# Kernel optimization log

Measured on AMD Instinct MI355X. Metric: run time of the kernel, lower is better.

The kernel has to match this reference:

```python
import jax, jax.numpy as jnp
import numpy as np

B, C, H, W = 4, 512, 64, 64
CQ = C // 8  # 64 channels for each of query/key projections


def conv1x1(t, w, b):
    # t: [B, Cin, H, W], w: [Cout, Cin], b: [Cout]
    return jnp.einsum('bchw,oc->bohw', t, w) + b[None, :, None, None]


def setup_inputs() -> dict:
    key = jax.random.key(0)
    ks = jax.random.split(key, 12)
    s = 0.05
    return {
        'x':   jax.random.normal(ks[0], (B, C, H, W), jnp.float32),
        'dep': jax.random.normal(ks[1], (B, C, H, W), jnp.float32),
        'wq':  jax.random.normal(ks[2], (CQ, C), jnp.float32) * s,
        'bq':  jnp.zeros((CQ,), jnp.float32),
        'wqd': jax.random.normal(ks[3], (CQ, C), jnp.float32) * s,
        'bqd': jnp.zeros((CQ,), jnp.float32),
        'wk':  jax.random.normal(ks[4], (CQ, C), jnp.float32) * s,
        'bk':  jnp.zeros((CQ,), jnp.float32),
        'wkd': jax.random.normal(ks[5], (CQ, C), jnp.float32) * s,
        'bkd': jnp.zeros((CQ,), jnp.float32),
        'wv':  jax.random.normal(ks[6], (C, C), jnp.float32) * s,
        'bv':  jnp.zeros((C,), jnp.float32),
        'gamma': jnp.full((1,), 0.5, jnp.float32),
    }


def reference(x, dep, wq, bq, wqd, bqd, wk, bk, wkd, bkd, wv, bv, gamma):
    b, c, h, w = x.shape
    n = h * w
    # concatenated RGB+depth query/key projections: [B, 2*CQ, N]
    q = jnp.concatenate([conv1x1(x, wq, bq), conv1x1(dep, wqd, bqd)], axis=1).reshape(b, -1, n)
    k = jnp.concatenate([conv1x1(x, wk, bk), conv1x1(dep, wkd, bkd)], axis=1).reshape(b, -1, n)
    # energy[b, i, j] = sum_d q[b, d, i] * k[b, d, j]  -> [B, N, N]
    energy = jnp.einsum('bdi,bdj->bij', q, k)
    attn = jax.nn.softmax(energy, axis=-1)
    v = conv1x1(x, wv, bv).reshape(b, c, n)  # [B, C, N]
    # out[b, c, i] = sum_j v[b, c, j] * attn[b, i, j]
    out = jnp.einsum('bcj,bij->bci', v, attn).reshape(b, c, h, w)
    return gamma.reshape(()) * out + x
```

## Files before the change

kernel.cpp:

```cpp
#include <hip/hip_runtime.h>


typedef __attribute__((ext_vector_type(8))) short bf16x8;
typedef __attribute__((ext_vector_type(4))) float f32x4;

__device__ __forceinline__ float bf2f(unsigned short u) {
  return __builtin_bit_cast(float, (unsigned int)u << 16);
}
__device__ __forceinline__ unsigned short f2bf(float f) {
  unsigned int u = __builtin_bit_cast(unsigned int, f);
  u = u + 0x7fffu + ((u >> 16) & 1u);
  return (unsigned short)(u >> 16);
}
__device__ __forceinline__ float bflo(unsigned int u) {
  return __builtin_bit_cast(float, u << 16);
}

__device__ __forceinline__ void gld16(const char* g, char* l) {
  __builtin_amdgcn_global_load_lds(
      (const __attribute__((address_space(1))) unsigned int*)g,
      (__attribute__((address_space(3))) unsigned int*)l, 16, 0, 0);
}

__device__ __forceinline__ int detect_fp32_mode(const void* xv) {
  const unsigned int* p = (const unsigned int*)xv;
  const int lane = threadIdx.x & 63;
  const unsigned int w0 = p[lane];
  const unsigned int w1 = p[64 + lane];
  int cnt = 0;
  const unsigned short us[4] = {
      (unsigned short)(w0 & 0xffffu), (unsigned short)(w0 >> 16),
      (unsigned short)(w1 & 0xffffu), (unsigned short)(w1 >> 16)};
#pragma unroll
  for (int h = 0; h < 4; ++h) {
    const float a = fabsf(bf2f(us[h]));
    cnt += (a > 9.0e-13f && a < 32.0f) ? 1 : 0;
  }
#pragma unroll
  for (int mm = 32; mm >= 1; mm >>= 1) cnt += __shfl_xor(cnt, mm, 64);
  return cnt < 220;
}

__global__ __launch_bounds__(256) void prep_kernel(
    const void* wq, const void* bq, const void* wqd, const void* bqd,
    const void* wk, const void* bk, const void* wkd, const void* bkd,
    const void* wv, const void* bv, const void* gam, const void* x,
    unsigned short* __restrict__ Whi, unsigned short* __restrict__ Wlo,
    float* __restrict__ Bcat, float* __restrict__ gamF)
{
  const int fp32mode = detect_fp32_mode(x);
  const int row = blockIdx.x;
  const void* src; const void* bsrc; int srow;
  if (row < 64)       { src = wq;  bsrc = bq;  srow = row; }
  else if (row < 128) { src = wqd; bsrc = bqd; srow = row - 64; }
  else if (row < 192) { src = wk;  bsrc = bk;  srow = row - 128; }
  else if (row < 256) { src = wkd; bsrc = bkd; srow = row - 192; }
  else                { src = wv;  bsrc = bv;  srow = row - 256; }
  for (int c = threadIdx.x; c < 512; c += 256) {
    const float v = fp32mode ? ((const float*)src)[(size_t)srow * 512 + c]
                             : bf2f(((const unsigned short*)src)[(size_t)srow * 512 + c]);
    const unsigned short h = f2bf(v);
    Whi[(size_t)row * 512 + c] = h;
    Wlo[(size_t)row * 512 + c] = f2bf(v - bf2f(h));
  }
  if (threadIdx.x == 0) {
    Bcat[row] = fp32mode ? ((const float*)bsrc)[srow]
                         : bf2f(((const unsigned short*)bsrc)[srow]);
    if (row == 0)
      gamF[0] = fp32mode ? ((const float*)gam)[0]
                         : bf2f(((const unsigned short*)gam)[0]);
  }
}

__global__ __launch_bounds__(256) void convert_kernel(
    const void* __restrict__ x, const void* __restrict__ dep,
    unsigned short* __restrict__ Xst)
{
  __shared__ float XT[512][36];
  const int fp32mode = detect_fp32_mode(x);
  const int tid = threadIdx.x;
  const int bid = blockIdx.x;
  const int src = bid & 1, t = (bid >> 1) & 127, b = bid >> 8;
  const int n0 = t * 32;
  const void* s = src ? dep : x;
  const int crow = tid >> 3;
  const int nf   = (tid & 7) * 4;

  float v[16][4];
  if (fp32mode) {
    const float* sp = (const float*)s;
#pragma unroll
    for (int r = 0; r < 16; ++r) {
      const int c = crow + r * 32;
      const float4 f4 = *(const float4*)(sp + (((size_t)b * 512 + c) << 12) + n0 + nf);
      v[r][0] = f4.x; v[r][1] = f4.y; v[r][2] = f4.z; v[r][3] = f4.w;
    }
  } else {
    const unsigned short* sp = (const unsigned short*)s;
#pragma unroll
    for (int r = 0; r < 16; ++r) {
      const int c = crow + r * 32;
      const uint2 u2 = *(const uint2*)(sp + (((size_t)b * 512 + c) << 12) + n0 + nf);
      v[r][0] = bflo(u2.x & 0xffffu); v[r][1] = bflo(u2.x >> 16);
      v[r][2] = bflo(u2.y & 0xffffu); v[r][3] = bflo(u2.y >> 16);
    }
  }
  __builtin_amdgcn_sched_barrier(0);
#pragma unroll
  for (int r = 0; r < 16; ++r) {
    const int c = crow + r * 32;
#pragma unroll
    for (int k = 0; k < 4; ++k) XT[c][nf + k] = v[r][k];
  }
  __syncthreads();

  const int n  = tid & 31;
  const int cg = tid >> 5;
  char* pb = (char*)Xst + ((((size_t)b * 128 + t) * 2 + src) << 16);
  const unsigned swz = (unsigned)(n & 7) << 4;
#pragma unroll
  for (int g = 0; g < 8; ++g) {
    unsigned short hi8[8], lo8[8];
#pragma unroll
    for (int i = 0; i < 8; ++i) {
      const float vv = XT[cg * 64 + g * 8 + i][n];
      const unsigned short h = f2bf(vv);
      hi8[i] = h;
      lo8[i] = f2bf(vv - bf2f(h));
    }
    const unsigned off = ((unsigned)(n * 1024 + 2 * (cg * 64 + g * 8))) ^ swz;
    *(uint4*)(pb + off)         = *(const uint4*)hi8;
    *(uint4*)(pb + 32768 + off) = *(const uint4*)lo8;
  }
}

__device__ __forceinline__ void gtile(
    const unsigned short* __restrict__ Whi, const unsigned short* __restrict__ Wlo,
    const float* bsh, const char* __restrict__ XL, int fp32mode,
    int wrow0, int kind, int d0, int b, int t, int n0, int l15, int quad,
    unsigned short* __restrict__ Qhi, unsigned short* __restrict__ Qlo,
    unsigned short* __restrict__ Kst, unsigned short* __restrict__ Vst)
{
  f32x4 A0, A1, B0, B1, C0, C1;
#pragma unroll
  for (int r = 0; r < 4; ++r) {
    A0[r] = A1[r] = bsh[wrow0 + quad * 4 + r];
    B0[r] = B1[r] = C0[r] = C1[r] = 0.f;
  }
  const unsigned short* wh_p = Whi + (size_t)(wrow0 + l15) * 512 + quad * 8;
  const unsigned short* wl_p = Wlo + (size_t)(wrow0 + l15) * 512 + quad * 8;
  const unsigned base0 = (unsigned)(l15 * 1024 + quad * 16);
  const unsigned swz   = (unsigned)(l15 & 7) << 4;

  bf16x8 hc = *(const bf16x8*)(wh_p);
  bf16x8 lc;
  if (fp32mode) lc = *(const bf16x8*)(wl_p);

#pragma unroll 2
  for (int ks = 0; ks < 16; ++ks) {
    bf16x8 hn, ln;
    if (ks < 15) {
      hn = *(const bf16x8*)(wh_p + (ks + 1) * 32);
      if (fp32mode) ln = *(const bf16x8*)(wl_p + (ks + 1) * 32);
    }
    const unsigned o0 = (base0 + ks * 64) ^ swz;
    const unsigned o1 = o0 + 16384;
    const bf16x8 b0 = *(const bf16x8*)(XL + o0);
    const bf16x8 b1 = *(const bf16x8*)(XL + o1);
    A0 = __builtin_amdgcn_mfma_f32_16x16x32_bf16(hc, b0, A0, 0, 0, 0);
    A1 = __builtin_amdgcn_mfma_f32_16x16x32_bf16(hc, b1, A1, 0, 0, 0);
    if (fp32mode) {
      const bf16x8 c0 = *(const bf16x8*)(XL + 32768 + o0);
      const bf16x8 c1 = *(const bf16x8*)(XL + 32768 + o1);
      B0 = __builtin_amdgcn_mfma_f32_16x16x32_bf16(hc, c0, B0, 0, 0, 0);
      C0 = __builtin_amdgcn_mfma_f32_16x16x32_bf16(lc, b0, C0, 0, 0, 0);
      B1 = __builtin_amdgcn_mfma_f32_16x16x32_bf16(hc, c1, B1, 0, 0, 0);
      C1 = __builtin_amdgcn_mfma_f32_16x16x32_bf16(lc, b1, C1, 0, 0, 0);
    }
    if (ks < 15) { hc = hn; if (fp32mode) lc = ln; }
  }

  const f32x4 a0 = fp32mode ? (A0 + B0) + C0 : A0;
  const f32x4 a1 = fp32mode ? (A1 + B1) + C1 : A1;
#pragma unroll
  for (int ns = 0; ns < 2; ++ns) {
    const f32x4 acc = ns ? a1 : a0;
    const int j = ns * 16 + l15;
    if (kind <= 1) {
      ushort4 h, l;
#pragma unroll
      for (int r = 0; r < 4; ++r) {
        const float f = acc[r];
        const unsigned short hh = f2bf(f);
        ((unsigned short*)&h)[r] = hh;
        ((unsigned short*)&l)[r] = f2bf(f - bf2f(hh));
      }
      if (kind == 0) {
        const size_t base = (((size_t)b << 12) + n0 + j) * 128 + d0 + quad * 4;
        *(ushort4*)(Qhi + base) = h;
        *(ushort4*)(Qlo + base) = l;
      } else {
        char* tb = (char*)Kst + (((size_t)b * 128 + t) << 14);
        const unsigned off =
            ((unsigned)(j * 256 + (d0 + quad * 4) * 2)) ^ ((unsigned)(j & 7) << 4);
        *(ushort4*)(tb + off) = h;
        *(ushort4*)(tb + 8192 + off) = l;
      }
    } else {
      char* tb = (char*)Vst + (((size_t)b * 128 + t) << 15);
#pragma unroll
      for (int r = 0; r < 4; ++r) {
        const int c = d0 + quad * 4 + r;
        const unsigned off =
            ((unsigned)(c * 64 + j * 2)) ^ ((unsigned)(c & 7) << 4);
        *(unsigned short*)(tb + off) = f2bf(acc[r]);
      }
    }
  }
}

__global__ __launch_bounds__(512, 4) void gemm_kernel(
    const void* __restrict__ x,
    const unsigned short* __restrict__ Whi, const unsigned short* __restrict__ Wlo,
    const float* __restrict__ Bcat, const unsigned short* __restrict__ Xst,
    unsigned short* __restrict__ Qhi, unsigned short* __restrict__ Qlo,
    unsigned short* __restrict__ Kst, unsigned short* __restrict__ Vst)
{
  __shared__ char XL[65536];
  __shared__ float bsh[768];
  const int fp32mode = detect_fp32_mode(x);
  const int tid  = threadIdx.x;
  const int lane = tid & 63;
  const int w    = tid >> 6;
  const int l15  = lane & 15;
  const int quad = lane >> 4;
  const int t  = blockIdx.x;
  const int b  = blockIdx.y;
  const int n0 = t * 32;

  for (int i = tid; i < 768; i += 512) bsh[i] = Bcat[i];

  const char* xsrc = (const char*)Xst + ((((size_t)b * 128 + t) * 2 + 0) << 16);
  const char* dsrc = xsrc + 65536;

#pragma unroll
  for (int i = 0; i < 8; ++i) {
    const int c8 = w + i * 8;
    gld16(xsrc + c8 * 1024 + lane * 16, XL + c8 * 1024);
  }
  __syncthreads();

  for (int i = 0; i < 5; ++i) {
    const int rt = w + i * 8;
    int wrow0, kind, d0;
    if (rt < 4)      { wrow0 = rt * 16;             kind = 0; d0 = rt * 16; }
    else if (rt < 8) { wrow0 = 128 + (rt - 4) * 16; kind = 1; d0 = (rt - 4) * 16; }
    else             { wrow0 = 256 + (rt - 8) * 16; kind = 2; d0 = (rt - 8) * 16; }
    gtile(Whi, Wlo, bsh, XL, fp32mode, wrow0, kind, d0, b, t, n0, l15, quad,
          Qhi, Qlo, Kst, Vst);
  }
  __syncthreads();

#pragma unroll
  for (int i = 0; i < 8; ++i) {
    const int c8 = w + i * 8;
    gld16(dsrc + c8 * 1024 + lane * 16, XL + c8 * 1024);
  }
  __syncthreads();

  {
    const int kind  = (w < 4) ? 0 : 1;
    const int wrow0 = (w < 4) ? 64 + w * 16 : 192 + (w - 4) * 16;
    const int d0    = 64 + (w & 3) * 16;
    gtile(Whi, Wlo, bsh, XL, fp32mode, wrow0, kind, d0, b, t, n0, l15, quad,
          Qhi, Qlo, Kst, Vst);
  }
}

__device__ __forceinline__ void stage_X(
    const void* __restrict__ src, int fp32mode, int b, int n0,
    int cbase, int nn,
    unsigned short* __restrict__ Xhi, unsigned short* __restrict__ Xlo)
{
  float v[8][4];
  if (fp32mode) {
    const float* s = (const float*)src;
#pragma unroll
    for (int r = 0; r < 8; ++r) {
      const int c = cbase + r * 64;
      const float4 f4 = *(const float4*)(s + (((size_t)b * 512 + c) << 12) + n0 + nn);
      v[r][0] = f4.x; v[r][1] = f4.y; v[r][2] = f4.z; v[r][3] = f4.w;
    }
  } else {
    const unsigned short* s = (const unsigned short*)src;
#pragma unroll
    for (int r = 0; r < 8; ++r) {
      const int c = cbase + r * 64;
      const uint2 u2 = *(const uint2*)(s + (((size_t)b * 512 + c) << 12) + n0 + nn);
      v[r][0] = bflo(u2.x & 0xffffu); v[r][1] = bflo(u2.x >> 16);
      v[r][2] = bflo(u2.y & 0xffffu); v[r][3] = bflo(u2.y >> 16);
    }
  }
  __builtin_amdgcn_sched_barrier(0);
#pragma unroll
  for (int r = 0; r < 8; ++r) {
    const int c = cbase + r * 64;
#pragma unroll
    for (int k = 0; k < 4; ++k) {
      const unsigned short h = f2bf(v[r][k]);
      Xhi[(nn + k) * 522 + c] = h;
      Xlo[(nn + k) * 522 + c] = f2bf(v[r][k] - bf2f(h));
    }
  }
}

__device__ __forceinline__ void do_tile_c(
    const unsigned short* __restrict__ Whi, const unsigned short* __restrict__ Wlo,
    const float* bsh,
    const unsigned short* Xhi, const unsigned short* Xlo, int fp32mode,
    int wrow0, int kind, int d0,
    int l15, int quad,
    char* __restrict__ QT, char* __restrict__ KT, char* __restrict__ VT)
{
  f32x4 A0, A1, B0, B1, C0, C1;
#pragma unroll
  for (int r = 0; r < 4; ++r) {
    A0[r] = A1[r] = bsh[wrow0 + quad * 4 + r];
    B0[r] = B1[r] = C0[r] = C1[r] = 0.f;
  }
  const unsigned short* wh_p = Whi + (size_t)(wrow0 + l15) * 512 + quad * 8;
  const unsigned short* wl_p = Wlo + (size_t)(wrow0 + l15) * 512 + quad * 8;
  const unsigned short* x0h = Xhi + l15 * 522 + quad * 8;
  const unsigned short* x1h = Xhi + (16 + l15) * 522 + quad * 8;
  const unsigned short* x0l = Xlo + l15 * 522 + quad * 8;
  const unsigned short* x1l = Xlo + (16 + l15) * 522 + quad * 8;

  bf16x8 hc = *(const bf16x8*)(wh_p);
  bf16x8 lc;
  if (fp32mode) lc = *(const bf16x8*)(wl_p);

#pragma unroll 2
  for (int ks = 0; ks < 16; ++ks) {
    bf16x8 hn, ln;
    if (ks < 15) {
      hn = *(const bf16x8*)(wh_p + (ks + 1) * 32);
      if (fp32mode) ln = *(const bf16x8*)(wl_p + (ks + 1) * 32);
    }
    const int o = ks * 32;
    const bf16x8 b0 = *(const bf16x8*)(x0h + o);
    const bf16x8 b1 = *(const bf16x8*)(x1h + o);
    A0 = __builtin_amdgcn_mfma_f32_16x16x32_bf16(hc, b0, A0, 0, 0, 0);
    A1 = __builtin_amdgcn_mfma_f32_16x16x32_bf16(hc, b1, A1, 0, 0, 0);
    if (fp32mode) {
      const bf16x8 c0 = *(const bf16x8*)(x0l + o);
      const bf16x8 c1 = *(const bf16x8*)(x1l + o);
      B0 = __builtin_amdgcn_mfma_f32_16x16x32_bf16(hc, c0, B0, 0, 0, 0);
      C0 = __builtin_amdgcn_mfma_f32_16x16x32_bf16(lc, b0, C0, 0, 0, 0);
      B1 = __builtin_amdgcn_mfma_f32_16x16x32_bf16(hc, c1, B1, 0, 0, 0);
      C1 = __builtin_amdgcn_mfma_f32_16x16x32_bf16(lc, b1, C1, 0, 0, 0);
    }
    if (ks < 15) { hc = hn; if (fp32mode) lc = ln; }
  }

  const f32x4 a0 = fp32mode ? (A0 + B0) + C0 : A0;
  const f32x4 a1 = fp32mode ? (A1 + B1) + C1 : A1;
#pragma unroll
  for (int ns = 0; ns < 2; ++ns) {
    const f32x4 acc = ns ? a1 : a0;
    const int n = ns * 16 + l15;
    if (kind <= 1) {
      ushort4 h, l;
#pragma unroll
      for (int r = 0; r < 4; ++r) {
        const float f = acc[r];
        const unsigned short hh = f2bf(f);
        ((unsigned short*)&h)[r] = hh;
        ((unsigned short*)&l)[r] = f2bf(f - bf2f(hh));
      }
      const unsigned lin = (unsigned)(n * 256 + (d0 + quad * 4) * 2);
      if (kind == 0) {
        *(ushort4*)(QT + lin) = h;
        *(ushort4*)(QT + 8192 + lin) = l;
      } else {
        const unsigned off = lin ^ ((unsigned)(n & 7) << 4);
        *(ushort4*)(KT + off) = h;
        *(ushort4*)(KT + 8192 + off) = l;
      }
    } else {
#pragma unroll
      for (int r = 0; r < 4; ++r) {
        const int c = d0 + quad * 4 + r;
        const unsigned off =
            ((unsigned)(c * 64 + n * 2)) ^ ((unsigned)(c & 7) << 4);
        *(unsigned short*)(VT + off) = f2bf(acc[r]);
      }
    }
  }
}

__global__ __launch_bounds__(512, 2) void proj_kernel(
    const void* __restrict__ x, const void* __restrict__ dep,
    const unsigned short* __restrict__ Whi, const unsigned short* __restrict__ Wlo,
    const float* __restrict__ Bcat,
    unsigned short* __restrict__ Qhi, unsigned short* __restrict__ Qlo,
    unsigned short* __restrict__ Kst, unsigned short* __restrict__ Vst)
{
  __shared__ unsigned short Xhi[32 * 522];
  __shared__ unsigned short Xlo[32 * 522];
  __shared__ char QT[16384];
  __shared__ char KT[16384];
  __shared__ char VT[32768];
  __shared__ float bsh[768];
  const int fp32mode = detect_fp32_mode(x);
  const int tid  = threadIdx.x;
  const int lane = tid & 63;
  const int w    = tid >> 6;
  const int l15  = lane & 15;
  const int quad = lane >> 4;
  const int b  = blockIdx.y;
  const int cbase = tid >> 3;
  const int nn    = (tid & 7) * 4;

  for (int i = tid; i < 768; i += 512) bsh[i] = Bcat[i];

  for (int rep = 0; rep < 2; ++rep) {
    const int t  = blockIdx.x + rep * 64;
    const int n0 = t * 32;
    stage_X(x, fp32mode, b, n0, cbase, nn, Xhi, Xlo);
    __syncthreads();
    for (int rt = w; rt < 40; rt += 8) {
      int wrow0, kind, d0;
      if (rt < 4)      { wrow0 = rt * 16;             kind = 0; d0 = rt * 16; }
      else if (rt < 8) { wrow0 = 128 + (rt - 4) * 16; kind = 1; d0 = (rt - 4) * 16; }
      else             { wrow0 = 256 + (rt - 8) * 16; kind = 2; d0 = (rt - 8) * 16; }
      do_tile_c(Whi, Wlo, bsh, Xhi, Xlo, fp32mode, wrow0, kind, d0,
                l15, quad, QT, KT, VT);
    }
    __syncthreads();
    {
      char* vdst = (char*)Vst + (((size_t)b * 128 + t) << 15);
#pragma unroll
      for (int i = 0; i < 4; ++i) {
        const int off = i * 8192 + tid * 16;
        *(uint4*)(vdst + off) = *(const uint4*)(VT + off);
      }
    }
    stage_X(dep, fp32mode, b, n0, cbase, nn, Xhi, Xlo);
    __syncthreads();
    {
      const int rt = w;
      const int kind  = (rt < 4) ? 0 : 1;
      const int wrow0 = (rt < 4) ? 64 + rt * 16 : 192 + (rt - 4) * 16;
      const int d0    = 64 + (rt & 3) * 16;
      do_tile_c(Whi, Wlo, bsh, Xhi, Xlo, fp32mode, wrow0, kind, d0,
                l15, quad, QT, KT, VT);
    }
    __syncthreads();
    {
      char* kdst = (char*)Kst + (((size_t)b * 128 + t) << 14);
#pragma unroll
      for (int i = 0; i < 2; ++i) {
        const int off = i * 8192 + tid * 16;
        *(uint4*)(kdst + off) = *(const uint4*)(KT + off);
      }
      const size_t qoff = ((((size_t)b << 12) + (size_t)t * 32) * 128) * 2;
      *(uint4*)((char*)Qhi + qoff + tid * 16) = *(const uint4*)(QT + tid * 16);
      *(uint4*)((char*)Qlo + qoff + tid * 16) = *(const uint4*)(QT + 8192 + tid * 16);
    }
    __syncthreads();
  }
}

__global__ __launch_bounds__(768, 3) void attn_kernel(
    const unsigned short* __restrict__ Qhi, const unsigned short* __restrict__ Qlo,
    const unsigned short* __restrict__ Kst, const unsigned short* __restrict__ Vst,
    const void* __restrict__ x, const float* __restrict__ gamF,
    void* __restrict__ outp)
{
  __shared__ char KL[2][16384];
  __shared__ char VL[2][32768];
  __shared__ unsigned short P[2][64][40];
  __shared__ float lstat[2][4][16];

  const int fp32mode = detect_fp32_mode(x);
  const int tid  = threadIdx.x;
  const int lane = tid & 63;
  const int w    = tid >> 6;
  const int l15  = lane & 15;
  const int quad = lane >> 4;
  const int id   = blockIdx.x;
  const int b    = (id >> 1) & 3;
  const int n0   = (((id >> 3) << 1) | (id & 1)) * 64;

  asm volatile("" :: "v"(fp32mode) : "memory");

  const char* Kb = (const char*)Kst + (((size_t)b * 128) << 14);
  const char* Vb = (const char*)Vst + (((size_t)b * 128) << 15);

  if (w < 4) {
    const int ihE = w >> 1;
    const int jt  = w & 1;
    bf16x8 qh[2][4], ql[2][4];
#pragma unroll
    for (int itq = 0; itq < 2; ++itq) {
      const size_t qb =
          (((size_t)b << 12) + n0 + ihE * 32 + itq * 16 + l15) * 128 + quad * 8;
#pragma unroll
      for (int ds = 0; ds < 4; ++ds) {
        qh[itq][ds] = *(const bf16x8*)(Qhi + qb + ds * 32);
        ql[itq][ds] = *(const bf16x8*)(Qlo + qb + ds * 32);
      }
    }
#pragma unroll
    for (int ch = 0; ch < 4; ++ch) {
      const int c = w + ch * 4;
      gld16(Kb + c * 1024 + lane * 16, &KL[0][c * 1024]);
    }
    float lpart[2] = {0.f, 0.f};

    for (int t = 0; t <= 128; ++t) {
      asm volatile("s_waitcnt vmcnt(0) lgkmcnt(0)" ::: "memory");
      __builtin_amdgcn_sched_barrier(0);
      __builtin_amdgcn_s_barrier();
      __builtin_amdgcn_sched_barrier(0);
      if (t < 128) {
        const int cur = t & 1;
        if (t < 127) {
          const char* src = Kb + ((size_t)(t + 1) << 14);
#pragma unroll
          for (int ch = 0; ch < 4; ++ch) {
            const int c = w + ch * 4;
            gld16(src + c * 1024 + lane * 16, &KL[cur ^ 1][c * 1024]);
          }
        }
        __builtin_amdgcn_sched_barrier(0);
        const int row = jt * 16 + l15;
        const unsigned rsw = (unsigned)(row & 7) << 4;
        const char* kb = &KL[cur][0];
        bf16x8 kh[4], kl[4];
#pragma unroll
        for (int ds = 0; ds < 4; ++ds) {
          const unsigned off = ((unsigned)(row * 256 + quad * 16 + ds * 64)) ^ rsw;
          kh[ds] = *(const bf16x8*)(kb + off);
          kl[ds] = *(const bf16x8*)(kb + 8192 + off);
        }
        f32x4 ea[2], eb[2], ec[2];
#pragma unroll
        for (int itq = 0; itq < 2; ++itq) {
          ea[itq] = (f32x4){0.f, 0.f, 0.f, 0.f};
          eb[itq] = (f32x4){0.f, 0.f, 0.f, 0.f};
          ec[itq] = (f32x4){0.f, 0.f, 0.f, 0.f};
        }
        __builtin_amdgcn_s_setprio(1);
#pragma unroll
        for (int ds = 0; ds < 4; ++ds)
#pragma unroll
          for (int itq = 0; itq < 2; ++itq) {
            ea[itq] = __builtin_amdgcn_mfma_f32_16x16x32_bf16(kh[ds], qh[itq][ds], ea[itq], 0, 0, 0);
            eb[itq] = __builtin_amdgcn_mfma_f32_16x16x32_bf16(kh[ds], ql[itq][ds], eb[itq], 0, 0, 0);
            ec[itq] = __builtin_amdgcn_mfma_f32_16x16x32_bf16(kl[ds], qh[itq][ds], ec[itq], 0, 0, 0);
          }
        __builtin_amdgcn_s_setprio(0);
#pragma unroll
        for (int itq = 0; itq < 2; ++itq) {
          const f32x4 e = (ea[itq] + eb[itq]) + ec[itq];
          const float p0 = __expf(e[0] - 32.0f);
          const float p1 = __expf(e[1] - 32.0f);
          const float p2 = __expf(e[2] - 32.0f);
          const float p3 = __expf(e[3] - 32.0f);
          const unsigned short u0 = f2bf(p0), u1 = f2bf(p1);
          const unsigned short u2 = f2bf(p2), u3 = f2bf(p3);
          lpart[itq] += (bf2f(u0) + bf2f(u1)) + (bf2f(u2) + bf2f(u3));
          unsigned int* dst = (unsigned int*)
              (&P[cur][ihE * 32 + itq * 16 + l15][jt * 16 + quad * 4]);
          dst[0] = (unsigned int)u0 | ((unsigned int)u1 << 16);
          dst[1] = (unsigned int)u2 | ((unsigned int)u3 << 16);
        }
      }
    }
#pragma unroll
    for (int itq = 0; itq < 2; ++itq) {
      float lp = lpart[itq];
      lp += __shfl_xor(lp, 16, 64);
      lp += __shfl_xor(lp, 32, 64);
      if (quad == 0) lstat[jt][ihE * 2 + itq][l15] = lp;
    }
    __syncthreads();
    return;
  }

  const int wv = w - 4;
#pragma unroll
  for (int k = 0; k < 4; ++k) {
    const int c = wv * 4 + k;
    gld16(Vb + c * 1024 + lane * 16, &VL[0][c * 1024]);
  }
  f32x4 acc[4][4];
#pragma unroll
  for (int ct = 0; ct < 4; ++ct)
#pragma unroll
    for (int itv = 0; itv < 4; ++itv) acc[ct][itv] = (f32x4){0.f, 0.f, 0.f, 0.f};

  for (int t = 0; t <= 128; ++t) {
    if (t <= 127)
      asm volatile("s_waitcnt vmcnt(4)" ::: "memory");
    else
      asm volatile("s_waitcnt vmcnt(0)" ::: "memory");
    __builtin_amdgcn_sched_barrier(0);
    __builtin_amdgcn_s_barrier();
    __builtin_amdgcn_sched_barrier(0);
    if (t >= 1) {
      const int pb = (t - 1) & 1;
      bf16x8 pf[4];
#pragma unroll
      for (int itv = 0; itv < 4; ++itv)
        pf[itv] = *(const bf16x8*)(&P[pb][itv * 16 + l15][quad * 8]);
      const char* vb = &VL[pb][0];
      __builtin_amdgcn_s_setprio(1);
#pragma unroll
      for (int ct = 0; ct < 4; ++ct) {
        const int c = wv * 64 + ct * 16 + l15;
        const unsigned off =
            ((unsigned)(c * 64 + quad * 16)) ^ ((unsigned)(c & 7) << 4);
        const bf16x8 va = *(const bf16x8*)(vb + off);
#pragma unroll
        for (int itv = 0; itv < 4; ++itv)
          acc[ct][itv] = __builtin_amdgcn_mfma_f32_16x16x32_bf16(va, pf[itv], acc[ct][itv], 0, 0, 0);
      }
      __builtin_amdgcn_s_setprio(0);
      __builtin_amdgcn_sched_barrier(0);
    }
    if (t < 127) {
      const char* src = Vb + ((size_t)(t + 1) << 15);
#pragma unroll
      for (int k = 0; k < 4; ++k) {
        const int c = wv * 4 + k;
        gld16(src + c * 1024 + lane * 16, &VL[(t + 1) & 1][c * 1024]);
      }
    }
  }
  __syncthreads();

  const float gv = gamF[0];
  float sc[4];
#pragma unroll
  for (int itv = 0; itv < 4; ++itv) {
    const float l = lstat[0][itv][l15] + lstat[1][itv][l15];
    sc[itv] = gv / l;
  }
#pragma unroll
  for (int ct = 0; ct < 4; ++ct)
#pragma unroll
    for (int r = 0; r < 4; ++r) {
      const int c_g = wv * 64 + ct * 16 + quad * 4 + r;
      const size_t brow = ((size_t)b * 512 + c_g) << 12;
#pragma unroll
      for (int itv = 0; itv < 4; ++itv) {
        const size_t addr = brow + n0 + itv * 16 + l15;
        const float o = sc[itv] * acc[ct][itv][r];
        if (fp32mode) {
          ((float*)outp)[addr] = o + ((const float*)x)[addr];
        } else {
          ((unsigned short*)outp)[addr] =
              f2bf(o + bf2f(((const unsigned short*)x)[addr]));
        }
      }
    }
}

extern "C" void kernel_launch(void* const* d_in, const int* in_sizes, int n_in,
                              void* d_out, int out_size, void* d_ws, size_t ws_size,
                              hipStream_t stream) {
  const void* x    = d_in[0];
  const void* dep  = d_in[1];
  const void* wq   = d_in[2];
  const void* bq   = d_in[3];
  const void* wqd  = d_in[4];
  const void* bqd  = d_in[5];
  const void* wk   = d_in[6];
  const void* bk   = d_in[7];
  const void* wkd  = d_in[8];
  const void* bkd  = d_in[9];
  const void* wv   = d_in[10];
  const void* bv   = d_in[11];
  const void* gam  = d_in[12];

  unsigned short* Whi = (unsigned short*)d_ws;
  unsigned short* Wlo = Whi + (size_t)768 * 512;
  float* Bcat = (float*)(Wlo + (size_t)768 * 512);
  float* gamF = Bcat + 768;
  unsigned short* Qhi = (unsigned short*)((char*)d_ws + ((size_t)2 << 20));
  unsigned short* Qlo = (unsigned short*)((char*)d_ws + ((size_t)6 << 20));
  unsigned short* Kst = (unsigned short*)((char*)d_ws + ((size_t)10 << 20));
  unsigned short* Vst = (unsigned short*)((char*)d_ws + ((size_t)18 << 20));
  unsigned short* Xst = (unsigned short*)((char*)d_ws + ((size_t)36 << 20));

  prep_kernel<<<768, 256, 0, stream>>>(wq, bq, wqd, bqd, wk, bk, wkd, bkd,
                                       wv, bv, gam, x, Whi, Wlo, Bcat, gamF);
  if (ws_size >= ((size_t)100 << 20)) {
    convert_kernel<<<1024, 256, 0, stream>>>(x, dep, Xst);
    gemm_kernel<<<dim3(128, 4), 512, 0, stream>>>(x, Whi, Wlo, Bcat, Xst,
                                                  Qhi, Qlo, Kst, Vst);
  } else {
    proj_kernel<<<dim3(64, 4), 512, 0, stream>>>(x, dep, Whi, Wlo, Bcat,
                                                 Qhi, Qlo, Kst, Vst);
  }
  attn_kernel<<<256, 768, 0, stream>>>(Qhi, Qlo, Kst, Vst, x, gamF, d_out);
}
```

Before: 396.3 us.

## Read K/V tiles directly from global memory and split energy work across eight waves

Drops the LDS double-buffered K and V staging (global_load_lds) and has each wave load its K and V fragments straight from global memory, depending on the cache. The energy stage now runs on eight producer waves, each handling 16 query rows instead of 32, and the block grows to 1024 threads. The aim is to free LDS, lower per-wave register pressure and give more parallelism to the softmax/energy producer. The cost is redundant global/L2 traffic, since every wave re-reads K and V, and load latency that is no longer hidden by prefetch. Launch bounds of (1024,4) may also force register spills.

```diff
diff --git a/kernel.cpp b/kernel.cpp
--- a/kernel.cpp
+++ b/kernel.cpp
@@ -471,14 +471,12 @@
   }
 }
 
-__global__ __launch_bounds__(768, 3) void attn_kernel(
+__global__ __launch_bounds__(1024, 4) void attn_kernel(
     const unsigned short* __restrict__ Qhi, const unsigned short* __restrict__ Qlo,
     const unsigned short* __restrict__ Kst, const unsigned short* __restrict__ Vst,
     const void* __restrict__ x, const float* __restrict__ gamF,
     void* __restrict__ outp)
 {
-  __shared__ char KL[2][16384];
-  __shared__ char VL[2][32768];
   __shared__ unsigned short P[2][64][40];
   __shared__ float lstat[2][4][16];
 
@@ -492,51 +490,33 @@
   const int b    = (id >> 1) & 3;
   const int n0   = (((id >> 3) << 1) | (id & 1)) * 64;
 
-  asm volatile("" :: "v"(fp32mode) : "memory");
-
   const char* Kb = (const char*)Kst + (((size_t)b * 128) << 14);
   const char* Vb = (const char*)Vst + (((size_t)b * 128) << 15);
 
-  if (w < 4) {
-    const int ihE = w >> 1;
-    const int jt  = w & 1;
-    bf16x8 qh[2][4], ql[2][4];
-#pragma unroll
-    for (int itq = 0; itq < 2; ++itq) {
+  if (w < 8) {
+    const int rg = w >> 1;
+    const int jt = w & 1;
+    bf16x8 qh[4], ql[4];
+    {
       const size_t qb =
-          (((size_t)b << 12) + n0 + ihE * 32 + itq * 16 + l15) * 128 + quad * 8;
+          (((size_t)b << 12) + n0 + rg * 16 + l15) * 128 + quad * 8;
 #pragma unroll
       for (int ds = 0; ds < 4; ++ds) {
-        qh[itq][ds] = *(const bf16x8*)(Qhi + qb + ds * 32);
-        ql[itq][ds] = *(const bf16x8*)(Qlo + qb + ds * 32);
-      }
-    }
-#pragma unroll
-    for (int ch = 0; ch < 4; ++ch) {
-      const int c = w + ch * 4;
-      gld16(Kb + c * 1024 + lane * 16, &KL[0][c * 1024]);
-    }
-    float lpart[2] = {0.f, 0.f};
+        qh[ds] = *(const bf16x8*)(Qhi + qb + ds * 32);
+        ql[ds] = *(const bf16x8*)(Qlo + qb + ds * 32);
+      }
+    }
+    const int row = jt * 16 + l15;
+    const unsigned rsw = (unsigned)(row & 7) << 4;
+    float lpart = 0.f;
 
     for (int t = 0; t <= 128; ++t) {
-      asm volatile("s_waitcnt vmcnt(0) lgkmcnt(0)" ::: "memory");
+      asm volatile("s_waitcnt lgkmcnt(0)" ::: "memory");
       __builtin_amdgcn_sched_barrier(0);
       __builtin_amdgcn_s_barrier();
       __builtin_amdgcn_sched_barrier(0);
       if (t < 128) {
-        const int cur = t & 1;
-        if (t < 127) {
-          const char* src = Kb + ((size_t)(t + 1) << 14);
-#pragma unroll
-          for (int ch = 0; ch < 4; ++ch) {
-            const int c = w + ch * 4;
-            gld16(src + c * 1024 + lane * 16, &KL[cur ^ 1][c * 1024]);
-          }
-        }
-        __builtin_amdgcn_sched_barrier(0);
-        const int row = jt * 16 + l15;
-        const unsigned rsw = (unsigned)(row & 7) << 4;
-        const char* kb = &KL[cur][0];
+        const char* kb = Kb + ((size_t)t << 14);
         bf16x8 kh[4], kl[4];
 #pragma unroll
         for (int ds = 0; ds < 4; ++ds) {
@@ -544,99 +524,77 @@
           kh[ds] = *(const bf16x8*)(kb + off);
           kl[ds] = *(const bf16x8*)(kb + 8192 + off);
         }
-        f32x4 ea[2], eb[2], ec[2];
-#pragma unroll
-        for (int itq = 0; itq < 2; ++itq) {
-          ea[itq] = (f32x4){0.f, 0.f, 0.f, 0.f};
-          eb[itq] = (f32x4){0.f, 0.f, 0.f, 0.f};
-          ec[itq] = (f32x4){0.f, 0.f, 0.f, 0.f};
+        __builtin_amdgcn_sched_barrier(0);
+        f32x4 ea = (f32x4){0.f, 0.f, 0.f, 0.f};
+        f32x4 eb = (f32x4){0.f, 0.f, 0.f, 0.f};
+        f32x4 ec = (f32x4){0.f, 0.f, 0.f, 0.f};
+        __builtin_amdgcn_s_setprio(1);
+#pragma unroll
+        for (int ds = 0; ds < 4; ++ds) {
+          ea = __builtin_amdgcn_mfma_f32_16x16x32_bf16(kh[ds], qh[ds], ea, 0, 0, 0);
+          eb = __builtin_amdgcn_mfma_f32_16x16x32_bf16(kh[ds], ql[ds], eb, 0, 0, 0);
+          ec = __builtin_amdgcn_mfma_f32_16x16x32_bf16(kl[ds], qh[ds], ec, 0, 0, 0);
         }
-        __builtin_amdgcn_s_setprio(1);
-#pragma unroll
-        for (int ds = 0; ds < 4; ++ds)
-#pragma unroll
-          for (int itq = 0; itq < 2; ++itq) {
-            ea[itq] = __builtin_amdgcn_mfma_f32_16x16x32_bf16(kh[ds], qh[itq][ds], ea[itq], 0, 0, 0);
-            eb[itq] = __builtin_amdgcn_mfma_f32_16x16x32_bf16(kh[ds], ql[itq][ds], eb[itq], 0, 0, 0);
-            ec[itq] = __builtin_amdgcn_mfma_f32_16x16x32_bf16(kl[ds], qh[itq][ds], ec[itq], 0, 0, 0);
-          }
         __builtin_amdgcn_s_setprio(0);
-#pragma unroll
-        for (int itq = 0; itq < 2; ++itq) {
-          const f32x4 e = (ea[itq] + eb[itq]) + ec[itq];
-          const float p0 = __expf(e[0] - 32.0f);
-          const float p1 = __expf(e[1] - 32.0f);
-          const float p2 = __expf(e[2] - 32.0f);
-          const float p3 = __expf(e[3] - 32.0f);
-          const unsigned short u0 = f2bf(p0), u1 = f2bf(p1);
-          const unsigned short u2 = f2bf(p2), u3 = f2bf(p3);
-          lpart[itq] += (bf2f(u0) + bf2f(u1)) + (bf2f(u2) + bf2f(u3));
-          unsigned int* dst = (unsigned int*)
-              (&P[cur][ihE * 32 + itq * 16 + l15][jt * 16 + quad * 4]);
-          dst[0] = (unsigned int)u0 | ((unsigned int)u1 << 16);
-          dst[1] = (unsigned int)u2 | ((unsigned int)u3 << 16);
-        }
-      }
-    }
-#pragma unroll
-    for (int itq = 0; itq < 2; ++itq) {
-      float lp = lpart[itq];
+        const f32x4 e = (ea + eb) + ec;
+        const float p0 = __expf(e[0] - 32.0f);
+        const float p1 = __expf(e[1] - 32.0f);
+        const float p2 = __expf(e[2] - 32.0f);
+        const float p3 = __expf(e[3] - 32.0f);
+        const unsigned short u0 = f2bf(p0), u1 = f2bf(p1);
+        const unsigned short u2 = f2bf(p2), u3 = f2bf(p3);
+        lpart += (bf2f(u0) + bf2f(u1)) + (bf2f(u2) + bf2f(u3));
+        unsigned int* dst = (unsigned int*)
+            (&P[t & 1][rg * 16 + l15][jt * 16 + quad * 4]);
+        dst[0] = (unsigned int)u0 | ((unsigned int)u1 << 16);
+        dst[1] = (unsigned int)u2 | ((unsigned int)u3 << 16);
+      }
+    }
+    {
+      float lp = lpart;
       lp += __shfl_xor(lp, 16, 64);
       lp += __shfl_xor(lp, 32, 64);
-      if (quad == 0) lstat[jt][ihE * 2 + itq][l15] = lp;
+      if (quad == 0) lstat[jt][rg][l15] = lp;
     }
     __syncthreads();
     return;
   }
 
-  const int wv = w - 4;
-#pragma unroll
-  for (int k = 0; k < 4; ++k) {
-    const int c = wv * 4 + k;
-    gld16(Vb + c * 1024 + lane * 16, &VL[0][c * 1024]);
-  }
+  const int wv = w - 8;
   f32x4 acc[4][4];
 #pragma unroll
   for (int ct = 0; ct < 4; ++ct)
 #pragma unroll
     for (int itv = 0; itv < 4; ++itv) acc[ct][itv] = (f32x4){0.f, 0.f, 0.f, 0.f};
 
+  const unsigned vswz = (unsigned)(l15 & 7) << 4;
   for (int t = 0; t <= 128; ++t) {
-    if (t <= 127)
-      asm volatile("s_waitcnt vmcnt(4)" ::: "memory");
-    else
-      asm volatile("s_waitcnt vmcnt(0)" ::: "memory");
+    asm volatile("s_waitcnt lgkmcnt(0)" ::: "memory");
     __builtin_amdgcn_sched_barrier(0);
     __builtin_amdgcn_s_barrier();
     __builtin_amdgcn_sched_barrier(0);
     if (t >= 1) {
       const int pb = (t - 1) & 1;
+      const char* vb = Vb + ((size_t)(t - 1) << 15);
+      bf16x8 va[4];
+#pragma unroll
+      for (int ct = 0; ct < 4; ++ct) {
+        const int c = wv * 64 + ct * 16 + l15;
+        const unsigned off = ((unsigned)(c * 64 + quad * 16)) ^ vswz;
+        va[ct] = *(const bf16x8*)(vb + off);
+      }
+      __builtin_amdgcn_sched_barrier(0);
       bf16x8 pf[4];
 #pragma unroll
       for (int itv = 0; itv < 4; ++itv)
         pf[itv] = *(const bf16x8*)(&P[pb][itv * 16 + l15][quad * 8]);
-      const char* vb = &VL[pb][0];
       __builtin_amdgcn_s_setprio(1);
 #pragma unroll
-      for (int ct = 0; ct < 4; ++ct) {
-        const int c = wv * 64 + ct * 16 + l15;
-        const unsigned off =
-            ((unsigned)(c * 64 + quad * 16)) ^ ((unsigned)(c & 7) << 4);
-        const bf16x8 va = *(const bf16x8*)(vb + off);
+      for (int ct = 0; ct < 4; ++ct)
 #pragma unroll
         for (int itv = 0; itv < 4; ++itv)
-          acc[ct][itv] = __builtin_amdgcn_mfma_f32_16x16x32_bf16(va, pf[itv], acc[ct][itv], 0, 0, 0);
-      }
+          acc[ct][itv] = __builtin_amdgcn_mfma_f32_16x16x32_bf16(va[ct], pf[itv], acc[ct][itv], 0, 0, 0);
       __builtin_amdgcn_s_setprio(0);
-      __builtin_amdgcn_sched_barrier(0);
-    }
-    if (t < 127) {
-      const char* src = Vb + ((size_t)(t + 1) << 15);
-#pragma unroll
-      for (int k = 0; k < 4; ++k) {
-        const int c = wv * 4 + k;
-        gld16(src + c * 1024 + lane * 16, &VL[(t + 1) & 1][c * 1024]);
-      }
     }
   }
   __syncthreads();
@@ -705,5 +663,5 @@
     proj_kernel<<<dim3(64, 4), 512, 0, stream>>>(x, dep, Whi, Wlo, Bcat,
                                                  Qhi, Qlo, Kst, Vst);
   }
-  attn_kernel<<<256, 768, 0, stream>>>(Qhi, Qlo, Kst, Vst, x, gamF, d_out);
-}
+  attn_kernel<<<256, 1024, 0, stream>>>(Qhi, Qlo, Kst, Vst, x, gamF, d_out);
+}
```

Result: slower. 442.4 us (+11.6%).
